# Kernel tuning notes

Hardware: AMD Instinct MI355X
Metric: run time of the kernel (lower is better)

## Reference

```python
import jax, jax.numpy as jnp
import numpy as np

# Static hypernetwork layer sizes from HyperOption(z_dim=256, inner_h=64, a_dim=32, layers=3)
SIZES = [256 * 64, 64, 64 * 64, 64, 64 * 32, 32]  # sum = 22688
SPLITS = np.cumsum(SIZES)[:-1]


def setup_inputs() -> dict:
    key = jax.random.key(0)
    ks = jax.random.split(key, 8)
    B, Z, H = 4096, 256, 1024
    return {
        "inputs": jax.random.normal(ks[0], (B, Z), dtype=jnp.float32),
        "option": jax.random.normal(ks[1], (B, sum(SIZES)), dtype=jnp.float32) * 0.05,
        "w1": jax.random.normal(ks[2], (H, Z), dtype=jnp.float32) * 0.05,
        "b1": jax.random.normal(ks[3], (H,), dtype=jnp.float32) * 0.05,
        "w2": jax.random.normal(ks[4], (H, H), dtype=jnp.float32) * 0.05,
        "b2": jax.random.normal(ks[5], (H,), dtype=jnp.float32) * 0.05,
        "w3": jax.random.normal(ks[6], (1, H), dtype=jnp.float32) * 0.05,
        "b3": jax.random.normal(ks[7], (1,), dtype=jnp.float32) * 0.05,
    }


def _apply_option(state, option):
    # Per-sample hypernetwork MLP: weights/biases packed in `option`.
    parts = jnp.split(option, SPLITS, axis=-1)
    cur = state
    n_layers = len(parts) // 2
    for i in range(n_layers):
        w = parts[2 * i].reshape(option.shape[0], -1, cur.shape[-1])  # [B, out, in]
        b = parts[2 * i + 1]                                          # [B, out]
        cur = jnp.einsum('boi,bi->bo', w, cur) + b
        if i < n_layers - 1:
            cur = jax.nn.relu(cur)
    return cur


def _value(z, w1, b1, w2, b2, w3, b3):
    t = jax.nn.elu(z @ w1.T + b1)
    t = jax.nn.elu(t @ w2.T + b2)
    return t @ w3.T + b3  # [B, 1]


def reference(inputs, option, w1, b1, w2, b2, w3, b3):
    value = _value(inputs, w1, b1, w2, b2, w3, b3)   # [B, 1]
    action = _apply_option(inputs, option)            # [B, 32]
    return jnp.concatenate([value, action], axis=-1)  # [B, 33]
```

## Files before the change

### kernel.cpp

```cpp
#include <hip/hip_runtime.h>
#include <hip/hip_bf16.h>
#include <cstdint>

typedef __attribute__((ext_vector_type(8))) short  short8;
typedef __attribute__((ext_vector_type(8))) __bf16 bf16x8;
typedef __attribute__((ext_vector_type(4))) float  floatx4;
typedef __attribute__((ext_vector_type(4))) short  short4v;

union Frag { short8 s; bf16x8 b; };

__device__ inline short f2bf(float f) {
    union { float f; unsigned u; } v; v.f = f;
    unsigned r = (v.u + 0x7fffu + ((v.u >> 16) & 1u)) >> 16;
    return (short)r;
}
__device__ inline float elu(float x) { return x > 0.f ? x : __expf(x) - 1.f; }

__device__ inline short8 load8_f32_to_bf16(const float* __restrict__ p) {
    float4 f0 = ((const float4*)p)[0];
    float4 f1 = ((const float4*)p)[1];
    short8 r;
    r[0] = f2bf(f0.x); r[1] = f2bf(f0.y); r[2] = f2bf(f0.z); r[3] = f2bf(f0.w);
    r[4] = f2bf(f1.x); r[5] = f2bf(f1.y); r[6] = f2bf(f1.z); r[7] = f2bf(f1.w);
    return r;
}

#define B_SZ   4096
#define Z_DIM  256
#define H_DIM  1024
#define OUT_W  33
#define OFF_W1 0
#define OFF_B1 16384
#define OFF_W2 16448
#define OFF_B2 20544
#define OFF_W3 20608
#define OFF_B3 22656
#define OPT_W  22688

#define HYP_K1 1024
#define G_BLOCKS 256
#define CONV_BLOCKS 64

template<int KTOT, bool ACONV, bool BCONV, bool VEPI>
__device__ __forceinline__ void gemm_tile(
    const void* __restrict__ Av, const void* __restrict__ Bv,
    const float* __restrict__ bias, const float* __restrict__ w3,
    __hip_bfloat16* __restrict__ T, float* __restrict__ out,
    int bm, int bn, int tid)
{
    const int lane = tid & 63, wid = tid >> 6;
    const int wm = wid >> 1, wn = wid & 1;
    const int m_wave = bm * 128 + wm * 64;
    const int n_wave = bn * 128 + wn * 64;
    const int lr = lane & 15, lk = (lane >> 4) * 8;

    floatx4 acc[4][4] = {};
    for (int k0 = 0; k0 < KTOT; k0 += 32) {
        Frag a[4], bb[4];
#pragma unroll
        for (int sm = 0; sm < 4; ++sm) {
            const size_t off = (size_t)(m_wave + sm * 16 + lr) * KTOT + k0 + lk;
            if constexpr (ACONV) a[sm].s = load8_f32_to_bf16((const float*)Av + off);
            else                 a[sm].s = *(const short8*)((const ushort*)Av + off);
        }
#pragma unroll
        for (int sn = 0; sn < 4; ++sn) {
            const size_t off = (size_t)(n_wave + sn * 16 + lr) * KTOT + k0 + lk;
            if constexpr (BCONV) bb[sn].s = load8_f32_to_bf16((const float*)Bv + off);
            else                 bb[sn].s = *(const short8*)((const ushort*)Bv + off);
        }
#pragma unroll
        for (int sm = 0; sm < 4; ++sm)
#pragma unroll
            for (int sn = 0; sn < 4; ++sn)
                acc[sm][sn] = __builtin_amdgcn_mfma_f32_16x16x32_bf16(
                    a[sm].b, bb[sn].b, acc[sm][sn], 0, 0, 0);
    }

    if constexpr (VEPI) {
        float bias_v[4], w3_v[4];
#pragma unroll
        for (int sn = 0; sn < 4; ++sn) {
            const int n = n_wave + sn * 16 + lr;
            bias_v[sn] = bias[n];
            w3_v[sn]   = w3[n];
        }
#pragma unroll
        for (int sm = 0; sm < 4; ++sm) {
#pragma unroll
            for (int r = 0; r < 4; ++r) {
                float rowsum = 0.f;
#pragma unroll
                for (int sn = 0; sn < 4; ++sn)
                    rowsum += elu(acc[sm][sn][r] + bias_v[sn]) * w3_v[sn];
                rowsum += __shfl_xor(rowsum, 1);
                rowsum += __shfl_xor(rowsum, 2);
                rowsum += __shfl_xor(rowsum, 4);
                rowsum += __shfl_xor(rowsum, 8);
                if (lr == 0) {
                    const int m = m_wave + sm * 16 + (lane >> 4) * 4 + r;
                    atomicAdd(out + (size_t)m * OUT_W, rowsum);
                }
            }
        }
    } else {
#pragma unroll
        for (int sm = 0; sm < 4; ++sm)
#pragma unroll
            for (int sn = 0; sn < 4; ++sn) {
                const int n = n_wave + sn * 16 + lr;
                const float bv = bias[n];
#pragma unroll
                for (int r = 0; r < 4; ++r) {
                    const int m = m_wave + sm * 16 + (lane >> 4) * 4 + r;
                    T[(size_t)m * H_DIM + n] = __float2bfloat16(elu(acc[sm][sn][r] + bv));
                }
            }
    }
}

__device__ __forceinline__ void hyper_sample(
    const float* __restrict__ z, const float* __restrict__ opt,
    float* __restrict__ out, int b, int tid,
    float* __restrict__ h1, float* __restrict__ h2)
{
    const int lane = tid & 63, w = tid >> 6;
    const float* __restrict__ orow = opt + (size_t)b * OPT_W;

    const float4 z4 = *(const float4*)(z + (size_t)b * Z_DIM + 4 * lane);

    {
        const float4* wbase = (const float4*)(orow + OFF_W1 + w * 16 * Z_DIM);
        float4 wv[16];
#pragma unroll
        for (int j = 0; j < 16; ++j) wv[j] = wbase[j * 64 + lane];
#pragma unroll
        for (int j = 0; j < 16; ++j) {
            float p = wv[j].x * z4.x + wv[j].y * z4.y + wv[j].z * z4.z + wv[j].w * z4.w;
            p += __shfl_xor(p, 1);  p += __shfl_xor(p, 2);
            p += __shfl_xor(p, 4);  p += __shfl_xor(p, 8);
            p += __shfl_xor(p, 16); p += __shfl_xor(p, 32);
            if (lane == 0) {
                const int r = 16 * w + j;
                h1[r] = fmaxf(p + orow[OFF_B1 + r], 0.f);
            }
        }
    }
    __syncthreads();

    {
        const float4 h1v = *(const float4*)(h1 + 4 * (lane & 15));
        const float4* wbase = (const float4*)(orow + OFF_W2 + w * 16 * 64);
        float4 wv[4];
#pragma unroll
        for (int j = 0; j < 4; ++j) wv[j] = wbase[j * 64 + lane];
#pragma unroll
        for (int j = 0; j < 4; ++j) {
            float p = wv[j].x * h1v.x + wv[j].y * h1v.y + wv[j].z * h1v.z + wv[j].w * h1v.w;
            p += __shfl_xor(p, 1); p += __shfl_xor(p, 2);
            p += __shfl_xor(p, 4); p += __shfl_xor(p, 8);
            if ((lane & 15) == 0) {
                const int r = 16 * w + j * 4 + (lane >> 4);
                h2[r] = fmaxf(p + orow[OFF_B2 + r], 0.f);
            }
        }
    }
    __syncthreads();

    {
        const float4 h2v = *(const float4*)(h2 + 4 * (lane & 15));
        const float4* wbase = (const float4*)(orow + OFF_W3 + w * 8 * 64);
        float4 wv[2];
#pragma unroll
        for (int j = 0; j < 2; ++j) wv[j] = wbase[j * 64 + lane];
#pragma unroll
        for (int j = 0; j < 2; ++j) {
            float p = wv[j].x * h2v.x + wv[j].y * h2v.y + wv[j].z * h2v.z + wv[j].w * h2v.w;
            p += __shfl_xor(p, 1); p += __shfl_xor(p, 2);
            p += __shfl_xor(p, 4); p += __shfl_xor(p, 8);
            if ((lane & 15) == 0) {
                const int r = 8 * w + j * 4 + (lane >> 4);
                out[(size_t)b * OUT_W + 1 + r] = p + orow[OFF_B3 + r];
            }
        }
    }
}

__global__ __launch_bounds__(256) void k1_kernel(
    const float* __restrict__ z, const float* __restrict__ opt,
    const float* __restrict__ w1, const float* __restrict__ b1,
    const float* __restrict__ w2, const float* __restrict__ b3,
    __hip_bfloat16* __restrict__ T1, __hip_bfloat16* __restrict__ w2bf,
    float* __restrict__ out)
{
    __shared__ float h1[64], h2[64];
    const int blk = blockIdx.x, t = threadIdx.x;

    if (blk < G_BLOCKS) {
        gemm_tile<Z_DIM, true, true, false>(z, w1, b1, nullptr, T1, nullptr,
                                            blk >> 3, blk & 7, t);
    } else if (blk < G_BLOCKS + CONV_BLOCKS) {
        const int gtid = (blk - G_BLOCKS) * 256 + t;
        if (gtid < B_SZ) out[(size_t)gtid * OUT_W] = b3[0];
#pragma unroll
        for (int i = 0; i < 16; ++i) {
            const int v = gtid + i * 16384;
            float4 f = ((const float4*)w2)[v];
            short4v s;
            s[0] = f2bf(f.x); s[1] = f2bf(f.y); s[2] = f2bf(f.z); s[3] = f2bf(f.w);
            ((short4v*)w2bf)[v] = s;
        }
    } else {
        hyper_sample(z, opt, out, blk - (G_BLOCKS + CONV_BLOCKS), t, h1, h2);
    }
}

__global__ __launch_bounds__(256) void k2_kernel(
    const float* __restrict__ z, const float* __restrict__ opt,
    const __hip_bfloat16* __restrict__ T1, const __hip_bfloat16* __restrict__ w2bf,
    const float* __restrict__ b2, const float* __restrict__ w3,
    float* __restrict__ out)
{
    __shared__ float h1[64], h2[64];
    const int blk = blockIdx.x, t = threadIdx.x;

    if (blk < G_BLOCKS) {
        gemm_tile<H_DIM, false, false, true>(T1, w2bf, b2, w3, nullptr, out,
                                             blk >> 3, blk & 7, t);
    } else {
        hyper_sample(z, opt, out, HYP_K1 + (blk - G_BLOCKS), t, h1, h2);
    }
}

extern "C" void kernel_launch(void* const* d_in, const int* in_sizes, int n_in,
                              void* d_out, int out_size, void* d_ws, size_t ws_size,
                              hipStream_t stream)
{
    const float* z   = (const float*)d_in[0];
    const float* opt = (const float*)d_in[1];
    const float* w1  = (const float*)d_in[2];
    const float* b1  = (const float*)d_in[3];
    const float* w2  = (const float*)d_in[4];
    const float* b2  = (const float*)d_in[5];
    const float* w3  = (const float*)d_in[6];
    const float* b3  = (const float*)d_in[7];
    float* out = (float*)d_out;

    __hip_bfloat16* T1   = (__hip_bfloat16*)d_ws;
    __hip_bfloat16* w2bf = (__hip_bfloat16*)((char*)d_ws +
                             (size_t)B_SZ * H_DIM * sizeof(__hip_bfloat16));

    k1_kernel<<<dim3(G_BLOCKS + CONV_BLOCKS + HYP_K1), dim3(256), 0, stream>>>(
        z, opt, w1, b1, w2, b3, T1, w2bf, out);

    k2_kernel<<<dim3(G_BLOCKS + (B_SZ - HYP_K1)), dim3(256), 0, stream>>>(
        z, opt, T1, w2bf, b2, w3, out);
}
```

Baseline: 137.9 us.

## Run hypernetwork per wave instead of per block, with nontemporal loads

Each hypernetwork sample is now handled by a single 64-lane wave rather than a 256-thread block, so the __syncthreads barriers go away and four samples share one block. The first-layer weight loads are double-buffered in registers, and streamed option data uses nontemporal loads to avoid polluting cache needed by the GEMM. The split of samples between the two kernels moves from 1024 to 1536. Each wave now holds more registers and carries a longer serial chain per sample, which may lower occupancy.

```diff
diff --git a/kernel.cpp b/kernel.cpp
--- a/kernel.cpp
+++ b/kernel.cpp
@@ -5,6 +5,7 @@
 typedef __attribute__((ext_vector_type(8))) short  short8;
 typedef __attribute__((ext_vector_type(8))) __bf16 bf16x8;
 typedef __attribute__((ext_vector_type(4))) float  floatx4;
+typedef __attribute__((ext_vector_type(4))) float  f32x4;
 typedef __attribute__((ext_vector_type(4))) short  short4v;
 
 union Frag { short8 s; bf16x8 b; };
@@ -23,6 +24,13 @@
     r[0] = f2bf(f0.x); r[1] = f2bf(f0.y); r[2] = f2bf(f0.z); r[3] = f2bf(f0.w);
     r[4] = f2bf(f1.x); r[5] = f2bf(f1.y); r[6] = f2bf(f1.z); r[7] = f2bf(f1.w);
     return r;
+}
+
+__device__ inline f32x4 ntload4(const f32x4* __restrict__ p) {
+    return __builtin_nontemporal_load(p);
+}
+__device__ inline float ntload1(const float* __restrict__ p) {
+    return __builtin_nontemporal_load(p);
 }
 
 #define B_SZ   4096
@@ -37,7 +45,7 @@
 #define OFF_B3 22656
 #define OPT_W  22688
 
-#define HYP_K1 1024
+#define HYP_K1 1536
 #define G_BLOCKS 256
 #define CONV_BLOCKS 64
 
@@ -119,69 +127,76 @@
     }
 }
 
-__device__ __forceinline__ void hyper_sample(
+__device__ __forceinline__ void hyper_wave(
     const float* __restrict__ z, const float* __restrict__ opt,
-    float* __restrict__ out, int b, int tid,
+    float* __restrict__ out, int b, int lane,
     float* __restrict__ h1, float* __restrict__ h2)
 {
-    const int lane = tid & 63, w = tid >> 6;
     const float* __restrict__ orow = opt + (size_t)b * OPT_W;
 
-    const float4 z4 = *(const float4*)(z + (size_t)b * Z_DIM + 4 * lane);
+    const f32x4 z4 = *(const f32x4*)(z + (size_t)b * Z_DIM + 4 * lane);
 
     {
-        const float4* wbase = (const float4*)(orow + OFF_W1 + w * 16 * Z_DIM);
-        float4 wv[16];
-#pragma unroll
-        for (int j = 0; j < 16; ++j) wv[j] = wbase[j * 64 + lane];
+        const f32x4* W = (const f32x4*)(orow + OFF_W1);
+        f32x4 wa[16], wb[16];
+#pragma unroll
+        for (int j = 0; j < 16; ++j) wa[j] = ntload4(W + j * 64 + lane);
+#pragma unroll
+        for (int c = 0; c < 4; ++c) {
+            f32x4* cur = (c & 1) ? wb : wa;
+            f32x4* nxt = (c & 1) ? wa : wb;
+            if (c < 3) {
+#pragma unroll
+                for (int j = 0; j < 16; ++j)
+                    nxt[j] = ntload4(W + ((c + 1) * 16 + j) * 64 + lane);
+            }
+#pragma unroll
+            for (int j = 0; j < 16; ++j) {
+                float p = cur[j].x * z4.x + cur[j].y * z4.y +
+                          cur[j].z * z4.z + cur[j].w * z4.w;
+                p += __shfl_xor(p, 1);  p += __shfl_xor(p, 2);
+                p += __shfl_xor(p, 4);  p += __shfl_xor(p, 8);
+                p += __shfl_xor(p, 16); p += __shfl_xor(p, 32);
+                const int r = c * 16 + j;
+                if (lane == 0)
+                    h1[r] = fmaxf(p + ntload1(orow + OFF_B1 + r), 0.f);
+            }
+        }
+    }
+
+    {
+        const f32x4 h1v = *(const f32x4*)(h1 + 4 * (lane & 15));
+        const f32x4* W = (const f32x4*)(orow + OFF_W2);
+        f32x4 wv[16];
+#pragma unroll
+        for (int j = 0; j < 16; ++j) wv[j] = ntload4(W + j * 64 + lane);
 #pragma unroll
         for (int j = 0; j < 16; ++j) {
-            float p = wv[j].x * z4.x + wv[j].y * z4.y + wv[j].z * z4.z + wv[j].w * z4.w;
-            p += __shfl_xor(p, 1);  p += __shfl_xor(p, 2);
-            p += __shfl_xor(p, 4);  p += __shfl_xor(p, 8);
-            p += __shfl_xor(p, 16); p += __shfl_xor(p, 32);
-            if (lane == 0) {
-                const int r = 16 * w + j;
-                h1[r] = fmaxf(p + orow[OFF_B1 + r], 0.f);
-            }
-        }
-    }
-    __syncthreads();
-
-    {
-        const float4 h1v = *(const float4*)(h1 + 4 * (lane & 15));
-        const float4* wbase = (const float4*)(orow + OFF_W2 + w * 16 * 64);
-        float4 wv[4];
-#pragma unroll
-        for (int j = 0; j < 4; ++j) wv[j] = wbase[j * 64 + lane];
-#pragma unroll
-        for (int j = 0; j < 4; ++j) {
-            float p = wv[j].x * h1v.x + wv[j].y * h1v.y + wv[j].z * h1v.z + wv[j].w * h1v.w;
+            float p = wv[j].x * h1v.x + wv[j].y * h1v.y +
+                      wv[j].z * h1v.z + wv[j].w * h1v.w;
             p += __shfl_xor(p, 1); p += __shfl_xor(p, 2);
             p += __shfl_xor(p, 4); p += __shfl_xor(p, 8);
-            if ((lane & 15) == 0) {
-                const int r = 16 * w + j * 4 + (lane >> 4);
-                h2[r] = fmaxf(p + orow[OFF_B2 + r], 0.f);
-            }
-        }
-    }
-    __syncthreads();
+            const int r = j * 4 + (lane >> 4);
+            if ((lane & 15) == 0)
+                h2[r] = fmaxf(p + ntload1(orow + OFF_B2 + r), 0.f);
+        }
+    }
 
     {
-        const float4 h2v = *(const float4*)(h2 + 4 * (lane & 15));
-        const float4* wbase = (const float4*)(orow + OFF_W3 + w * 8 * 64);
-        float4 wv[2];
-#pragma unroll
-        for (int j = 0; j < 2; ++j) wv[j] = wbase[j * 64 + lane];
-#pragma unroll
-        for (int j = 0; j < 2; ++j) {
-            float p = wv[j].x * h2v.x + wv[j].y * h2v.y + wv[j].z * h2v.z + wv[j].w * h2v.w;
+        const f32x4 h2v = *(const f32x4*)(h2 + 4 * (lane & 15));
+        const f32x4* W = (const f32x4*)(orow + OFF_W3);
+        f32x4 wv[8];
+#pragma unroll
+        for (int j = 0; j < 8; ++j) wv[j] = ntload4(W + j * 64 + lane);
+#pragma unroll
+        for (int j = 0; j < 8; ++j) {
+            float p = wv[j].x * h2v.x + wv[j].y * h2v.y +
+                      wv[j].z * h2v.z + wv[j].w * h2v.w;
             p += __shfl_xor(p, 1); p += __shfl_xor(p, 2);
             p += __shfl_xor(p, 4); p += __shfl_xor(p, 8);
-            if ((lane & 15) == 0) {
-                const int r = 8 * w + j * 4 + (lane >> 4);
-                out[(size_t)b * OUT_W + 1 + r] = p + orow[OFF_B3 + r];
-            }
+            const int r = j * 4 + (lane >> 4);
+            if ((lane & 15) == 0)
+                out[(size_t)b * OUT_W + 1 + r] = p + ntload1(orow + OFF_B3 + r);
         }
     }
 }
@@ -193,7 +208,7 @@
     __hip_bfloat16* __restrict__ T1, __hip_bfloat16* __restrict__ w2bf,
     float* __restrict__ out)
 {
-    __shared__ float h1[64], h2[64];
+    __shared__ float hbuf[4][128];
     const int blk = blockIdx.x, t = threadIdx.x;
 
     if (blk < G_BLOCKS) {
@@ -211,7 +226,9 @@
             ((short4v*)w2bf)[v] = s;
         }
     } else {
-        hyper_sample(z, opt, out, blk - (G_BLOCKS + CONV_BLOCKS), t, h1, h2);
+        const int wid = t >> 6, lane = t & 63;
+        const int b = (blk - (G_BLOCKS + CONV_BLOCKS)) * 4 + wid;
+        hyper_wave(z, opt, out, b, lane, hbuf[wid], hbuf[wid] + 64);
     }
 }
 
@@ -221,14 +238,16 @@
     const float* __restrict__ b2, const float* __restrict__ w3,
     float* __restrict__ out)
 {
-    __shared__ float h1[64], h2[64];
+    __shared__ float hbuf[4][128];
     const int blk = blockIdx.x, t = threadIdx.x;
 
     if (blk < G_BLOCKS) {
         gemm_tile<H_DIM, false, false, true>(T1, w2bf, b2, w3, nullptr, out,
                                              blk >> 3, blk & 7, t);
     } else {
-        hyper_sample(z, opt, out, HYP_K1 + (blk - G_BLOCKS), t, h1, h2);
+        const int wid = t >> 6, lane = t & 63;
+        const int b = HYP_K1 + (blk - G_BLOCKS) * 4 + wid;
+        hyper_wave(z, opt, out, b, lane, hbuf[wid], hbuf[wid] + 64);
     }
 }
 
@@ -250,9 +269,9 @@
     __hip_bfloat16* w2bf = (__hip_bfloat16*)((char*)d_ws +
                              (size_t)B_SZ * H_DIM * sizeof(__hip_bfloat16));
 
-    k1_kernel<<<dim3(G_BLOCKS + CONV_BLOCKS + HYP_K1), dim3(256), 0, stream>>>(
+    k1_kernel<<<dim3(G_BLOCKS + CONV_BLOCKS + HYP_K1 / 4), dim3(256), 0, stream>>>(
         z, opt, w1, b1, w2, b3, T1, w2bf, out);
 
-    k2_kernel<<<dim3(G_BLOCKS + (B_SZ - HYP_K1)), dim3(256), 0, stream>>>(
+    k2_kernel<<<dim3(G_BLOCKS + (B_SZ - HYP_K1) / 4), dim3(256), 0, stream>>>(
         z, opt, T1, w2bf, b2, w3, out);
 }
```

Result: slower. 186.3 us (+35.1%).
